# Kernel optimization log

Measured on AMD Instinct MI355X. Metric: run time of the kernel, lower is better.

Reference implementation:

```python
import jax, jax.numpy as jnp
import numpy as np

LAMBDA_U = 0.01
LAMBDA_V = 0.01
PRED_DIMS = 4  # predict() gathers only latent dims [0,1,2,3] even though latent_size=5


def setup_inputs() -> dict:
    key = jax.random.key(0)
    k_u, k_v, k_r, k_ui, k_vi = jax.random.split(key, 5)
    NU = 12000   # num_users
    NI = 12000   # num_items
    L = 5        # latent_size
    NP = 1000000 # number of (user, item) prediction pairs
    U = jax.random.uniform(k_u, (NU, L), dtype=jnp.float32)
    V = jax.random.uniform(k_v, (NI, L), dtype=jnp.float32)
    R = jax.random.uniform(k_r, (NU, NI), dtype=jnp.float32)
    u_idx = jax.random.randint(k_ui, (NP,), 0, NU, dtype=jnp.int64 if jax.config.jax_enable_x64 else jnp.int32)
    v_idx = jax.random.randint(k_vi, (NP,), 0, NI, dtype=jnp.int64 if jax.config.jax_enable_x64 else jnp.int32)
    return {"U": U, "V": V, "R": R, "u_idx": u_idx, "v_idx": v_idx}


def reference(U, V, R, u_idx, v_idx):
    # PMF.loss(): I masks observed ratings (I = 1 where R != 0)
    I = (R != 0).astype(R.dtype)
    err = R - jnp.matmul(U, V.T)                      # [NU, NI]
    loss = jnp.sum(I * err * err) \
         + LAMBDA_U * jnp.sum(U * U) \
         + LAMBDA_V * jnp.sum(V * V)
    # PMF.predict(): batched row gather + elementwise mul + sum over first 4 dims
    u_feat = U[u_idx, :PRED_DIMS]                     # [NP, 4]
    v_feat = V[v_idx, :PRED_DIMS]                     # [NP, 4]
    preds = jnp.sum(u_feat * v_feat, axis=1)          # [NP]
    return (loss, preds)
```

## Files before the change

kernel.cpp:

```cpp
#include <hip/hip_runtime.h>
#include <cstdint>

static constexpr int NU = 12000;
static constexpr int NI = 12000;
static constexpr int L  = 5;
static constexpr int PRED_DIMS = 4;
static constexpr float LAMBDA = 0.01f;

static constexpr int CGRP = NI / 4;
static constexpr int NR_SPLIT = 128;
static constexpr int MAIN_THREADS = CGRP * NR_SPLIT;
static constexpr int MAIN_BLOCKS  = MAIN_THREADS / 256;
static constexpr int REG_BLOCKS = 64;

__global__ __launch_bounds__(256) void loss_main_kernel(
        const float* __restrict__ U, const float* __restrict__ V,
        const float* __restrict__ R, double* __restrict__ partial) {
    const int gid = blockIdx.x * 256 + threadIdx.x;
    const int c  = gid % CGRP;
    const int r0 = gid / CGRP;

    float vv[20];
    {
        const float4* vb = reinterpret_cast<const float4*>(V + 20 * (size_t)c);
#pragma unroll
        for (int k = 0; k < 5; ++k) {
            float4 t = vb[k];
            vv[4 * k + 0] = t.x; vv[4 * k + 1] = t.y;
            vv[4 * k + 2] = t.z; vv[4 * k + 3] = t.w;
        }
    }

    double acc = 0.0;
    const float4* Rp = reinterpret_cast<const float4*>(R) + (size_t)r0 * CGRP + c;
    const size_t rstride = (size_t)NR_SPLIT * CGRP;

    for (int i = r0; i < NU; i += NR_SPLIT) {
        const float4 rv = *Rp;
        const float* Urow = U + (size_t)i * L;
        const float u0 = Urow[0], u1 = Urow[1], u2 = Urow[2],
                    u3 = Urow[3], u4 = Urow[4];

        const float d0 = u0*vv[0]  + u1*vv[1]  + u2*vv[2]  + u3*vv[3]  + u4*vv[4];
        const float d1 = u0*vv[5]  + u1*vv[6]  + u2*vv[7]  + u3*vv[8]  + u4*vv[9];
        const float d2 = u0*vv[10] + u1*vv[11] + u2*vv[12] + u3*vv[13] + u4*vv[14];
        const float d3 = u0*vv[15] + u1*vv[16] + u2*vv[17] + u3*vv[18] + u4*vv[19];

        const float e0 = rv.x - d0;
        const float e1 = rv.y - d1;
        const float e2 = rv.z - d2;
        const float e3 = rv.w - d3;

        const float s = (rv.x != 0.0f ? e0 * e0 : 0.0f)
                      + (rv.y != 0.0f ? e1 * e1 : 0.0f)
                      + (rv.z != 0.0f ? e2 * e2 : 0.0f)
                      + (rv.w != 0.0f ? e3 * e3 : 0.0f);
        acc += (double)s;
        Rp += rstride;
    }

#pragma unroll
    for (int off = 32; off > 0; off >>= 1) acc += __shfl_down(acc, off);
    __shared__ double sacc[4];
    const int lane = threadIdx.x & 63, w = threadIdx.x >> 6;
    if (lane == 0) sacc[w] = acc;
    __syncthreads();
    if (threadIdx.x == 0)
        partial[blockIdx.x] = sacc[0] + sacc[1] + sacc[2] + sacc[3];
}

__global__ __launch_bounds__(256) void reg_kernel(
        const float* __restrict__ U, const float* __restrict__ V,
        double* __restrict__ partial_reg) {
    const int gid = blockIdx.x * 256 + threadIdx.x;
    const int n4 = (NU * L) / 4;
    double acc = 0.0;
    const float4* Uf = reinterpret_cast<const float4*>(U);
    const float4* Vf = reinterpret_cast<const float4*>(V);
    for (int k = gid; k < n4; k += REG_BLOCKS * 256) {
        float4 a = Uf[k];
        float4 b = Vf[k];
        acc += (double)(a.x*a.x + a.y*a.y + a.z*a.z + a.w*a.w
                      + b.x*b.x + b.y*b.y + b.z*b.z + b.w*b.w);
    }
#pragma unroll
    for (int off = 32; off > 0; off >>= 1) acc += __shfl_down(acc, off);
    __shared__ double sacc[4];
    const int lane = threadIdx.x & 63, w = threadIdx.x >> 6;
    if (lane == 0) sacc[w] = acc;
    __syncthreads();
    if (threadIdx.x == 0)
        partial_reg[blockIdx.x] = sacc[0] + sacc[1] + sacc[2] + sacc[3];
}

__global__ __launch_bounds__(256) void pred_kernel(
        const float* __restrict__ U, const float* __restrict__ V,
        const int* __restrict__ u_idx, const int* __restrict__ v_idx,
        float* __restrict__ out, int np) {
    const int p = blockIdx.x * 256 + threadIdx.x;
    if (p >= np) return;
    const int u = u_idx[p];
    const int v = v_idx[p];
    const float* up = U + (size_t)u * L;
    const float* vp = V + (size_t)v * L;
    out[1 + p] = up[0]*vp[0] + up[1]*vp[1] + up[2]*vp[2] + up[3]*vp[3];
}

__global__ __launch_bounds__(256) void finalize_kernel(
        const double* __restrict__ partial_main,
        const double* __restrict__ partial_reg,
        float* __restrict__ out) {
    double acc = 0.0;
    for (int k = threadIdx.x; k < MAIN_BLOCKS; k += 256) acc += partial_main[k];
    double reg = 0.0;
    for (int k = threadIdx.x; k < REG_BLOCKS; k += 256) reg += partial_reg[k];
    acc += (double)LAMBDA * reg;
#pragma unroll
    for (int off = 32; off > 0; off >>= 1) acc += __shfl_down(acc, off);
    __shared__ double sacc[4];
    const int lane = threadIdx.x & 63, w = threadIdx.x >> 6;
    if (lane == 0) sacc[w] = acc;
    __syncthreads();
    if (threadIdx.x == 0)
        out[0] = (float)(sacc[0] + sacc[1] + sacc[2] + sacc[3]);
}

extern "C" void kernel_launch(void* const* d_in, const int* in_sizes, int n_in,
                              void* d_out, int out_size, void* d_ws, size_t ws_size,
                              hipStream_t stream) {
    const float* U = (const float*)d_in[0];
    const float* V = (const float*)d_in[1];
    const float* R = (const float*)d_in[2];
    const int* u_idx = (const int*)d_in[3];
    const int* v_idx = (const int*)d_in[4];
    float* out = (float*)d_out;
    const int np = in_sizes[3];

    double* partial_main = (double*)d_ws;
    double* partial_reg  = partial_main + MAIN_BLOCKS;

    loss_main_kernel<<<MAIN_BLOCKS, 256, 0, stream>>>(U, V, R, partial_main);
    reg_kernel<<<REG_BLOCKS, 256, 0, stream>>>(U, V, partial_reg);
    pred_kernel<<<(np + 255) / 256, 256, 0, stream>>>(U, V, u_idx, v_idx, out, np);
    finalize_kernel<<<1, 256, 0, stream>>>(partial_main, partial_reg, out);
}
```

Before: 746.8 us.

## Fuse loss, prediction and regularisation kernels into one block-partitioned launch

Merges the loss, prediction-gather and regularisation kernels into a single launch whose blocks are split by index range, so the three independent jobs run concurrently and two launch gaps disappear. The loss loop now handles two rows per iteration with NR_SPLIT raised to 256, giving more loads in flight. Prediction threads each read four indices with int4 loads, and the regularisation block count is halved. In exchange the fused kernel's register use is set by its heaviest branch, and pred_blocks uses np/4 rounded down, so a tail of np not divisible by 4 would be skipped.

New measurement: 750.7 us. Within noise of the previous version (+0.5%).

```diff
diff --git a/kernel.cpp b/kernel.cpp
--- a/kernel.cpp
+++ b/kernel.cpp
@@ -4,106 +4,137 @@
 static constexpr int NU = 12000;
 static constexpr int NI = 12000;
 static constexpr int L  = 5;
-static constexpr int PRED_DIMS = 4;
 static constexpr float LAMBDA = 0.01f;
 
 static constexpr int CGRP = NI / 4;
-static constexpr int NR_SPLIT = 128;
-static constexpr int MAIN_THREADS = CGRP * NR_SPLIT;
-static constexpr int MAIN_BLOCKS  = MAIN_THREADS / 256;
-static constexpr int REG_BLOCKS = 64;
+static constexpr int NR_SPLIT = 256;
+static constexpr int LOSS_BLOCKS = CGRP * NR_SPLIT / 256;
+static constexpr int REG_BLOCKS = 32;
 
-__global__ __launch_bounds__(256) void loss_main_kernel(
+__global__ __launch_bounds__(256) void pmf_fused_kernel(
         const float* __restrict__ U, const float* __restrict__ V,
-        const float* __restrict__ R, double* __restrict__ partial) {
-    const int gid = blockIdx.x * 256 + threadIdx.x;
-    const int c  = gid % CGRP;
-    const int r0 = gid / CGRP;
+        const float* __restrict__ R,
+        const int* __restrict__ u_idx, const int* __restrict__ v_idx,
+        float* __restrict__ out, int np,
+        double* __restrict__ partial_main, double* __restrict__ partial_reg,
+        int pred_blocks) {
+    const int b = blockIdx.x;
 
-    float vv[20];
-    {
-        const float4* vb = reinterpret_cast<const float4*>(V + 20 * (size_t)c);
+    if (b < LOSS_BLOCKS) {
+        const int gid = b * 256 + threadIdx.x;
+        const int c  = gid % CGRP;
+        const int r0 = gid / CGRP;
+
+        float vv[20];
+        {
+            const float4* vb = reinterpret_cast<const float4*>(V + 20 * (size_t)c);
 #pragma unroll
-        for (int k = 0; k < 5; ++k) {
-            float4 t = vb[k];
-            vv[4 * k + 0] = t.x; vv[4 * k + 1] = t.y;
-            vv[4 * k + 2] = t.z; vv[4 * k + 3] = t.w;
+            for (int k = 0; k < 5; ++k) {
+                float4 t = vb[k];
+                vv[4*k+0] = t.x; vv[4*k+1] = t.y; vv[4*k+2] = t.z; vv[4*k+3] = t.w;
+            }
         }
-    }
 
-    double acc = 0.0;
-    const float4* Rp = reinterpret_cast<const float4*>(R) + (size_t)r0 * CGRP + c;
-    const size_t rstride = (size_t)NR_SPLIT * CGRP;
+        double acc = 0.0;
+        const size_t rstr = (size_t)NR_SPLIT * CGRP;
+        const float4* Rp = reinterpret_cast<const float4*>(R) + (size_t)r0 * CGRP + c;
+        int i = r0;
 
-    for (int i = r0; i < NU; i += NR_SPLIT) {
-        const float4 rv = *Rp;
-        const float* Urow = U + (size_t)i * L;
-        const float u0 = Urow[0], u1 = Urow[1], u2 = Urow[2],
-                    u3 = Urow[3], u4 = Urow[4];
+        for (; i + NR_SPLIT < NU; i += 2 * NR_SPLIT, Rp += 2 * rstr) {
+            const float4 ra = Rp[0];
+            const float4 rb = Rp[rstr];
+            const float* Ua = U + (size_t)i * L;
+            const float* Ub = U + (size_t)(i + NR_SPLIT) * L;
+            const float a0 = Ua[0], a1 = Ua[1], a2 = Ua[2], a3 = Ua[3], a4 = Ua[4];
+            const float b0 = Ub[0], b1 = Ub[1], b2 = Ub[2], b3 = Ub[3], b4 = Ub[4];
 
-        const float d0 = u0*vv[0]  + u1*vv[1]  + u2*vv[2]  + u3*vv[3]  + u4*vv[4];
-        const float d1 = u0*vv[5]  + u1*vv[6]  + u2*vv[7]  + u3*vv[8]  + u4*vv[9];
-        const float d2 = u0*vv[10] + u1*vv[11] + u2*vv[12] + u3*vv[13] + u4*vv[14];
-        const float d3 = u0*vv[15] + u1*vv[16] + u2*vv[17] + u3*vv[18] + u4*vv[19];
+            float da0 = a0*vv[0]  + a1*vv[1]  + a2*vv[2]  + a3*vv[3]  + a4*vv[4];
+            float da1 = a0*vv[5]  + a1*vv[6]  + a2*vv[7]  + a3*vv[8]  + a4*vv[9];
+            float da2 = a0*vv[10] + a1*vv[11] + a2*vv[12] + a3*vv[13] + a4*vv[14];
+            float da3 = a0*vv[15] + a1*vv[16] + a2*vv[17] + a3*vv[18] + a4*vv[19];
+            float db0 = b0*vv[0]  + b1*vv[1]  + b2*vv[2]  + b3*vv[3]  + b4*vv[4];
+            float db1 = b0*vv[5]  + b1*vv[6]  + b2*vv[7]  + b3*vv[8]  + b4*vv[9];
+            float db2 = b0*vv[10] + b1*vv[11] + b2*vv[12] + b3*vv[13] + b4*vv[14];
+            float db3 = b0*vv[15] + b1*vv[16] + b2*vv[17] + b3*vv[18] + b4*vv[19];
 
-        const float e0 = rv.x - d0;
-        const float e1 = rv.y - d1;
-        const float e2 = rv.z - d2;
-        const float e3 = rv.w - d3;
-
-        const float s = (rv.x != 0.0f ? e0 * e0 : 0.0f)
-                      + (rv.y != 0.0f ? e1 * e1 : 0.0f)
-                      + (rv.z != 0.0f ? e2 * e2 : 0.0f)
-                      + (rv.w != 0.0f ? e3 * e3 : 0.0f);
-        acc += (double)s;
-        Rp += rstride;
-    }
+            float e;
+            float s = 0.0f;
+            e = ra.x - da0; s += (ra.x != 0.0f) ? e*e : 0.0f;
+            e = ra.y - da1; s += (ra.y != 0.0f) ? e*e : 0.0f;
+            e = ra.z - da2; s += (ra.z != 0.0f) ? e*e : 0.0f;
+            e = ra.w - da3; s += (ra.w != 0.0f) ? e*e : 0.0f;
+            e = rb.x - db0; s += (rb.x != 0.0f) ? e*e : 0.0f;
+            e = rb.y - db1; s += (rb.y != 0.0f) ? e*e : 0.0f;
+            e = rb.z - db2; s += (rb.z != 0.0f) ? e*e : 0.0f;
+            e = rb.w - db3; s += (rb.w != 0.0f) ? e*e : 0.0f;
+            acc += (double)s;
+        }
+        if (i < NU) {
+            const float4 ra = Rp[0];
+            const float* Ua = U + (size_t)i * L;
+            const float a0 = Ua[0], a1 = Ua[1], a2 = Ua[2], a3 = Ua[3], a4 = Ua[4];
+            float da0 = a0*vv[0]  + a1*vv[1]  + a2*vv[2]  + a3*vv[3]  + a4*vv[4];
+            float da1 = a0*vv[5]  + a1*vv[6]  + a2*vv[7]  + a3*vv[8]  + a4*vv[9];
+            float da2 = a0*vv[10] + a1*vv[11] + a2*vv[12] + a3*vv[13] + a4*vv[14];
+            float da3 = a0*vv[15] + a1*vv[16] + a2*vv[17] + a3*vv[18] + a4*vv[19];
+            float e; float s = 0.0f;
+            e = ra.x - da0; s += (ra.x != 0.0f) ? e*e : 0.0f;
+            e = ra.y - da1; s += (ra.y != 0.0f) ? e*e : 0.0f;
+            e = ra.z - da2; s += (ra.z != 0.0f) ? e*e : 0.0f;
+            e = ra.w - da3; s += (ra.w != 0.0f) ? e*e : 0.0f;
+            acc += (double)s;
+        }
 
 #pragma unroll
-    for (int off = 32; off > 0; off >>= 1) acc += __shfl_down(acc, off);
-    __shared__ double sacc[4];
-    const int lane = threadIdx.x & 63, w = threadIdx.x >> 6;
-    if (lane == 0) sacc[w] = acc;
-    __syncthreads();
-    if (threadIdx.x == 0)
-        partial[blockIdx.x] = sacc[0] + sacc[1] + sacc[2] + sacc[3];
-}
+        for (int off = 32; off > 0; off >>= 1) acc += __shfl_down(acc, off);
+        __shared__ double sacc[4];
+        const int lane = threadIdx.x & 63, w = threadIdx.x >> 6;
+        if (lane == 0) sacc[w] = acc;
+        __syncthreads();
+        if (threadIdx.x == 0)
+            partial_main[b] = sacc[0] + sacc[1] + sacc[2] + sacc[3];
 
-__global__ __launch_bounds__(256) void reg_kernel(
-        const float* __restrict__ U, const float* __restrict__ V,
-        double* __restrict__ partial_reg) {
-    const int gid = blockIdx.x * 256 + threadIdx.x;
-    const int n4 = (NU * L) / 4;
-    double acc = 0.0;
-    const float4* Uf = reinterpret_cast<const float4*>(U);
-    const float4* Vf = reinterpret_cast<const float4*>(V);
-    for (int k = gid; k < n4; k += REG_BLOCKS * 256) {
-        float4 a = Uf[k];
-        float4 b = Vf[k];
-        acc += (double)(a.x*a.x + a.y*a.y + a.z*a.z + a.w*a.w
-                      + b.x*b.x + b.y*b.y + b.z*b.z + b.w*b.w);
+    } else if (b < LOSS_BLOCKS + pred_blocks) {
+        const int t = (b - LOSS_BLOCKS) * 256 + threadIdx.x;
+        const int base = t * 4;
+        if (base < np) {
+            const int4 ui = *reinterpret_cast<const int4*>(u_idx + base);
+            const int4 vi = *reinterpret_cast<const int4*>(v_idx + base);
+#pragma unroll
+            for (int k = 0; k < 4; ++k) {
+                const int p = base + k;
+                if (p < np) {
+                    const int u = (k == 0) ? ui.x : (k == 1) ? ui.y : (k == 2) ? ui.z : ui.w;
+                    const int v = (k == 0) ? vi.x : (k == 1) ? vi.y : (k == 2) ? vi.z : vi.w;
+                    const float* up = U + (size_t)u * L;
+                    const float* vp = V + (size_t)v * L;
+                    out[1 + p] = up[0]*vp[0] + up[1]*vp[1] + up[2]*vp[2] + up[3]*vp[3];
+                }
+            }
+        }
+
+    } else {
+        const int rb = b - LOSS_BLOCKS - pred_blocks;
+        const int gid = rb * 256 + threadIdx.x;
+        const int n4 = (NU * L) / 4;
+        double acc = 0.0;
+        const float4* Uf = reinterpret_cast<const float4*>(U);
+        const float4* Vf = reinterpret_cast<const float4*>(V);
+        for (int k = gid; k < n4; k += REG_BLOCKS * 256) {
+            float4 a = Uf[k];
+            float4 v = Vf[k];
+            acc += (double)(a.x*a.x + a.y*a.y + a.z*a.z + a.w*a.w
+                          + v.x*v.x + v.y*v.y + v.z*v.z + v.w*v.w);
+        }
+#pragma unroll
+        for (int off = 32; off > 0; off >>= 1) acc += __shfl_down(acc, off);
+        __shared__ double sacc[4];
+        const int lane = threadIdx.x & 63, w = threadIdx.x >> 6;
+        if (lane == 0) sacc[w] = acc;
+        __syncthreads();
+        if (threadIdx.x == 0)
+            partial_reg[rb] = sacc[0] + sacc[1] + sacc[2] + sacc[3];
     }
-#pragma unroll
-    for (int off = 32; off > 0; off >>= 1) acc += __shfl_down(acc, off);
-    __shared__ double sacc[4];
-    const int lane = threadIdx.x & 63, w = threadIdx.x >> 6;
-    if (lane == 0) sacc[w] = acc;
-    __syncthreads();
-    if (threadIdx.x == 0)
-        partial_reg[blockIdx.x] = sacc[0] + sacc[1] + sacc[2] + sacc[3];
-}
-
-__global__ __launch_bounds__(256) void pred_kernel(
-        const float* __restrict__ U, const float* __restrict__ V,
-        const int* __restrict__ u_idx, const int* __restrict__ v_idx,
-        float* __restrict__ out, int np) {
-    const int p = blockIdx.x * 256 + threadIdx.x;
-    if (p >= np) return;
-    const int u = u_idx[p];
-    const int v = v_idx[p];
-    const float* up = U + (size_t)u * L;
-    const float* vp = V + (size_t)v * L;
-    out[1 + p] = up[0]*vp[0] + up[1]*vp[1] + up[2]*vp[2] + up[3]*vp[3];
 }
 
 __global__ __launch_bounds__(256) void finalize_kernel(
@@ -111,7 +142,7 @@
         const double* __restrict__ partial_reg,
         float* __restrict__ out) {
     double acc = 0.0;
-    for (int k = threadIdx.x; k < MAIN_BLOCKS; k += 256) acc += partial_main[k];
+    for (int k = threadIdx.x; k < LOSS_BLOCKS; k += 256) acc += partial_main[k];
     double reg = 0.0;
     for (int k = threadIdx.x; k < REG_BLOCKS; k += 256) reg += partial_reg[k];
     acc += (double)LAMBDA * reg;
@@ -137,10 +168,12 @@
     const int np = in_sizes[3];
 
     double* partial_main = (double*)d_ws;
-    double* partial_reg  = partial_main + MAIN_BLOCKS;
+    double* partial_reg  = partial_main + LOSS_BLOCKS;
 
-    loss_main_kernel<<<MAIN_BLOCKS, 256, 0, stream>>>(U, V, R, partial_main);
-    reg_kernel<<<REG_BLOCKS, 256, 0, stream>>>(U, V, partial_reg);
-    pred_kernel<<<(np + 255) / 256, 256, 0, stream>>>(U, V, u_idx, v_idx, out, np);
+    const int pred_blocks = (np / 4 + 255) / 256;
+    const int total_blocks = LOSS_BLOCKS + pred_blocks + REG_BLOCKS;
+
+    pmf_fused_kernel<<<total_blocks, 256, 0, stream>>>(
+        U, V, R, u_idx, v_idx, out, np, partial_main, partial_reg, pred_blocks);
     finalize_kernel<<<1, 256, 0, stream>>>(partial_main, partial_reg, out);
 }
```
